# Optimization experiments

Hardware: AMD Instinct MI355X
Metric: run time of the kernel (lower is better)

## Reference

```python
import jax, jax.numpy as jnp
import numpy as np

N = 50000
E = 800000
F_IN = 256
HID = 64
HEADS = 4
CLASSES = 32
NEG_SLOPE = 0.2


def setup_inputs() -> dict:
    key = jax.random.key(0)
    ks = jax.random.split(key, 10)
    x = jax.random.normal(ks[0], (N, F_IN), dtype=jnp.float32)
    edge_index = jax.random.randint(ks[1], (2, E), 0, N, dtype=jnp.int64)
    s1 = 1.0 / np.sqrt(F_IN)
    s2 = 1.0 / np.sqrt(HID * HEADS)
    W1 = jax.random.normal(ks[2], (F_IN, HEADS * HID), dtype=jnp.float32) * s1
    a_src1 = jax.random.normal(ks[3], (HEADS, HID), dtype=jnp.float32) * s1
    a_dst1 = jax.random.normal(ks[4], (HEADS, HID), dtype=jnp.float32) * s1
    b1 = jnp.zeros((HEADS * HID,), dtype=jnp.float32)
    W2 = jax.random.normal(ks[5], (HEADS * HID, CLASSES), dtype=jnp.float32) * s2
    a_src2 = jax.random.normal(ks[6], (1, CLASSES), dtype=jnp.float32) * s2
    a_dst2 = jax.random.normal(ks[7], (1, CLASSES), dtype=jnp.float32) * s2
    b2 = jnp.zeros((CLASSES,), dtype=jnp.float32)
    return {"x": x, "edge_index": edge_index, "W1": W1, "a_src1": a_src1,
            "a_dst1": a_dst1, "b1": b1, "W2": W2, "a_src2": a_src2,
            "a_dst2": a_dst2, "b2": b2}


def gat_conv(x, src, dst, W, a_src, a_dst, bias, num_nodes):
    # PyG GATConv: h = x W, per-head attention logits, segment softmax over dst,
    # scatter-weighted aggregation. src/dst already include self-loops.
    H, C = a_src.shape
    h = (x @ W).reshape(num_nodes, H, C)               # [N, H, C]
    al_s = jnp.sum(h * a_src[None], axis=-1)            # [N, H]
    al_d = jnp.sum(h * a_dst[None], axis=-1)            # [N, H]
    e = jax.nn.leaky_relu(al_s[src] + al_d[dst], NEG_SLOPE)  # [Et, H]
    m = jax.ops.segment_max(e, dst, num_segments=num_nodes)  # [N, H]
    ex = jnp.exp(e - m[dst])
    denom = jax.ops.segment_sum(ex, dst, num_segments=num_nodes)
    alpha = ex / denom[dst]                              # [Et, H]
    out = jax.ops.segment_sum(alpha[:, :, None] * h[src], dst,
                              num_segments=num_nodes)    # [N, H, C]
    return out.reshape(num_nodes, H * C) + bias


def reference(x, edge_index, W1, a_src1, a_dst1, b1, W2, a_src2, a_dst2, b2):
    num_nodes = x.shape[0]
    loop = jnp.arange(num_nodes, dtype=edge_index.dtype)
    src = jnp.concatenate([edge_index[0], loop])  # add_self_loops=True (PyG default)
    dst = jnp.concatenate([edge_index[1], loop])
    # dropout is identity in eval mode
    h = jax.nn.elu(gat_conv(x, src, dst, W1, a_src1, a_dst1, b1, num_nodes))
    out = gat_conv(h, src, dst, W2, a_src2, a_dst2, b2, num_nodes)
    return jax.nn.log_softmax(out, axis=1)
```

## Files before the change

### kernel.cpp

```cpp
#include <hip/hip_runtime.h>
#include <math.h>

#define N_NODES 50000
#define N_EDGES 800000
#define NEG_SLOPE 0.2f
#define PADU N_NODES

#define BSHIFT 8
#define NBUK ((N_NODES + 255) >> BSHIFT)
#define BCAP 4608
#define ACHUNK 4096
#define ET_PAD_ALLOC 1000960

typedef __attribute__((ext_vector_type(8))) short s16x8;
typedef __attribute__((ext_vector_type(4))) float f32x4;
typedef __attribute__((ext_vector_type(2))) float f32x2;

__device__ __forceinline__ unsigned short f2bf(float f) {
    union { float f; unsigned u; } v; v.f = f;
    unsigned r = v.u + 0x7FFF + ((v.u >> 16) & 1);
    return (unsigned short)(r >> 16);
}
__device__ __forceinline__ float bf2f(unsigned short s) {
    union { unsigned u; float f; } v; v.u = ((unsigned)s) << 16;
    return v.f;
}
__device__ __forceinline__ uint4 pack_bf16_trunc(float4 f0, float4 f1) {
    const unsigned* a = (const unsigned*)&f0;
    const unsigned* b = (const unsigned*)&f1;
    uint4 r;
    r.x = (a[0] >> 16) | (a[1] & 0xffff0000u);
    r.y = (a[2] >> 16) | (a[3] & 0xffff0000u);
    r.z = (b[0] >> 16) | (b[1] & 0xffff0000u);
    r.w = (b[2] >> 16) | (b[3] & 0xffff0000u);
    return r;
}
__device__ __forceinline__ unsigned char f2fp8(float f) {
    return (unsigned char)(__builtin_amdgcn_cvt_pk_fp8_f32(f, f, 0, false) & 0xff);
}


__global__ __launch_bounds__(256) void k_cvtw(const float* __restrict__ W1, const float* __restrict__ W2,
                                              unsigned short* __restrict__ WT, unsigned short* __restrict__ W2T,
                                              int* __restrict__ bcur, float* __restrict__ als1) {
    int b = blockIdx.x, k = threadIdx.x;
    if (b < 256) {
        WT[b * 256 + k] = f2bf(W1[k * 256 + b]);
    } else if (b < 288) {
        int c = b - 256;
        W2T[c * 256 + k] = f2bf(W2[k * 32 + c]);
    } else {
        if (k < NBUK) bcur[k] = 0;
        if (k >= 196 && k < 200) als1[N_NODES * 4 + (k - 196)] = -1e30f;
    }
}


__global__ __launch_bounds__(256) void k_bin(const int* __restrict__ ei, int* __restrict__ bcur,
                                             unsigned* __restrict__ stage) {
    __shared__ unsigned sdata[ACHUNK];
    __shared__ unsigned short sv[ACHUNK];
    __shared__ int scnt[NBUK];
    __shared__ int soff[NBUK + 1];
    __shared__ int sgbase[NBUK];
    __shared__ int wssc[4];
    int tid = threadIdx.x;
    int e0 = blockIdx.x * ACHUNK;
    int nE = N_EDGES - e0;
    if (nE > ACHUNK) nE = ACHUNK;
    for (int i = tid; i < NBUK; i += 256) scnt[i] = 0;
    __syncthreads();
    for (int i = tid; i < nE; i += 256) {
        int v = ei[N_EDGES + e0 + i];
        sv[i] = (unsigned short)v;
        atomicAdd(&scnt[v >> BSHIFT], 1);
    }
    __syncthreads();
    {
        int lane = tid & 63, w = tid >> 6;
        int val = (tid < NBUK) ? scnt[tid] : 0;
        int incl = val;
        for (int o = 1; o < 64; o <<= 1) {
            int t = __shfl_up(incl, o);
            if (lane >= o) incl += t;
        }
        if (lane == 63) wssc[w] = incl;
        __syncthreads();
        int wb = 0;
        for (int i = 0; i < w; ++i) wb += wssc[i];
        if (tid < NBUK) soff[tid] = wb + incl - val;
        if (tid == 255) soff[NBUK] = wb + incl;
    }
    __syncthreads();
    if (tid < NBUK) {
        int c = scnt[tid];
        sgbase[tid] = c ? atomicAdd(&bcur[tid], c) : 0;
        scnt[tid] = soff[tid];
    }
    __syncthreads();
    for (int i = tid; i < nE; i += 256) {
        int u = ei[e0 + i];
        unsigned v = sv[i];
        int b = (int)(v >> BSHIFT);
        int pos = atomicAdd(&scnt[b], 1);
        sdata[pos] = (unsigned)u | ((v & 255u) << 16) | ((unsigned)b << 24);
    }
    __syncthreads();
    for (int i = tid; i < nE; i += 256) {
        unsigned pk = sdata[i];
        int buk = (int)(pk >> 24);
        int rel = sgbase[buk] + (i - soff[buk]);
        if (rel < BCAP) stage[(size_t)buk * BCAP + rel] = pk;
    }
}


__global__ __launch_bounds__(256) void k_bukscan(const int* __restrict__ bcur, int* __restrict__ bukbase) {
    __shared__ int ws[4];
    int tid = threadIdx.x, lane = tid & 63, w = tid >> 6;
    int val = 0;
    if (tid < NBUK) {
        int base = tid << BSHIFT;
        int nv = N_NODES - base;
        if (nv > 256) nv = 256;
        val = (bcur[tid] + 4 * nv + 3) & ~3;
    }
    int incl = val;
    for (int o = 1; o < 64; o <<= 1) {
        int t = __shfl_up(incl, o);
        if (lane >= o) incl += t;
    }
    if (lane == 63) ws[w] = incl;
    __syncthreads();
    int wb = 0;
    for (int i = 0; i < w; ++i) wb += ws[i];
    if (tid < NBUK) bukbase[tid] = wb + incl - val;
}


__global__ __launch_bounds__(256) void k_build(const unsigned* __restrict__ stage,
                                               const int* __restrict__ bcur, const int* __restrict__ bukbase,
                                               int* __restrict__ offp, int* __restrict__ ecnt,
                                               unsigned short* __restrict__ esrc) {
    __shared__ int hist[256];
    __shared__ int lexcl[257];
    __shared__ int ws[4];
    __shared__ int outbuf[5632];
    int b = blockIdx.x, tid = threadIdx.x;
    int n = bcur[b];
    if (n > BCAP) n = BCAP;
    int base = b << BSHIFT;
    int nv = N_NODES - base;
    if (nv > 256) nv = 256;
    hist[tid] = 0;
    __syncthreads();
    const unsigned* sg = stage + (size_t)b * BCAP;
    for (int i = tid; i < n; i += 256) atomicAdd(&hist[(sg[i] >> 16) & 0xFF], 1);
    __syncthreads();
    int lane = tid & 63, w = tid >> 6;
    int c = (tid < nv) ? hist[tid] + 1 : 0;
    int r = (tid < nv) ? ((c + 3) & ~3) : 0;
    int incl = r;
    for (int o = 1; o < 64; o <<= 1) {
        int t = __shfl_up(incl, o);
        if (lane >= o) incl += t;
    }
    if (lane == 63) ws[w] = incl;
    __syncthreads();
    int wb = 0;
    for (int i = 0; i < w; ++i) wb += ws[i];
    int excl = wb + incl - r;
    lexcl[tid] = excl;
    if (tid == 255) lexcl[256] = excl + r;
    int gb = bukbase[b];
    if (tid < nv) {
        offp[base + tid] = gb + excl;
        ecnt[base + tid] = c;
    }
    __syncthreads();
    int total = lexcl[256];
    if (tid < nv) {
        outbuf[excl] = base + tid;
        for (int j = excl + c; j < excl + r; ++j) outbuf[j] = PADU;
        hist[tid] = 1;
    }
    __syncthreads();
    for (int i = tid; i < n; i += 256) {
        unsigned pk = sg[i];
        int vloc = (int)((pk >> 16) & 0xFF);
        int pos = lexcl[vloc] + atomicAdd(&hist[vloc], 1);
        outbuf[pos] = (int)(pk & 0xffffu);
    }
    __syncthreads();
    for (int i = tid; i < total; i += 256) esrc[gb + i] = (unsigned short)outbuf[i];
}


__global__ __launch_bounds__(256) void k_gemm1m(const float* __restrict__ X, const unsigned short* __restrict__ WT,
                                                const float* __restrict__ a_src, const float* __restrict__ a_dst,
                                                unsigned char* __restrict__ H8,
                                                float* __restrict__ als, float* __restrict__ ald) {
    __shared__ unsigned short As[64][40];
    __shared__ unsigned short Bs[256][40];
    int tid = threadIdx.x;
    int row0 = blockIdx.x * 64;
    int wv = tid >> 6, lane = tid & 63;
    int wm = wv & 1, wn = wv >> 1;
    int lr = lane & 15, quad = lane >> 4;
    f32x4 acc[2][8];
#pragma unroll
    for (int mt = 0; mt < 2; ++mt)
#pragma unroll
        for (int nt = 0; nt < 8; ++nt) acc[mt][nt] = (f32x4){0.f, 0.f, 0.f, 0.f};

    int ar = tid >> 2, aseg = tid & 3;
    for (int k0 = 0; k0 < 256; k0 += 32) {
        {
            int grow = row0 + ar;
            float4 f0 = make_float4(0.f, 0.f, 0.f, 0.f), f1 = f0;
            if (grow < N_NODES) {
                const float* src = X + (size_t)grow * 256 + k0 + aseg * 8;
                f0 = *(const float4*)src;
                f1 = *(const float4*)(src + 4);
            }
            *(uint4*)&As[ar][aseg * 8] = pack_bf16_trunc(f0, f1);
        }
#pragma unroll
        for (int pass = 0; pass < 4; ++pass) {
            int q = tid + pass * 256;
            int n = q >> 2, seg = q & 3;
            uint4 v = *(const uint4*)(WT + (n << 8) + k0 + seg * 8);
            *(uint4*)&Bs[n][seg * 8] = v;
        }
        __syncthreads();
        s16x8 a[2], b[8];
#pragma unroll
        for (int mt = 0; mt < 2; ++mt) a[mt] = *(const s16x8*)&As[wm * 32 + mt * 16 + lr][quad * 8];
#pragma unroll
        for (int nt = 0; nt < 8; ++nt) b[nt] = *(const s16x8*)&Bs[wn * 128 + nt * 16 + lr][quad * 8];
#pragma unroll
        for (int mt = 0; mt < 2; ++mt)
#pragma unroll
            for (int nt = 0; nt < 8; ++nt)
                acc[mt][nt] = __builtin_amdgcn_mfma_f32_16x16x32_bf16(a[mt], b[nt], acc[mt][nt], 0, 0, 0);
        __syncthreads();
    }
#pragma unroll
    for (int mt = 0; mt < 2; ++mt) {
#pragma unroll
        for (int r = 0; r < 4; ++r) {
            int row = row0 + wm * 32 + mt * 16 + quad * 4 + r;
            if (row < N_NODES) {
#pragma unroll
                for (int nt = 0; nt < 8; ++nt) {
                    int col = wn * 128 + nt * 16 + lr;
                    H8[(size_t)row * 256 + col] = f2fp8(acc[mt][nt][r]);
                }
            }
        }
    }
    float av[8], dv[8];
#pragma unroll
    for (int nt = 0; nt < 8; ++nt) {
        int col = wn * 128 + nt * 16 + lr;
        av[nt] = a_src[col];
        dv[nt] = a_dst[col];
    }
    float ps[2][8], pd[2][8];
#pragma unroll
    for (int hl = 0; hl < 2; ++hl)
#pragma unroll
        for (int i = 0; i < 8; ++i) { ps[hl][i] = 0.f; pd[hl][i] = 0.f; }
#pragma unroll
    for (int mt = 0; mt < 2; ++mt)
#pragma unroll
        for (int nt = 0; nt < 8; ++nt) {
            int hl = nt >> 2;
#pragma unroll
            for (int r = 0; r < 4; ++r) {
                float v = acc[mt][nt][r];
                ps[hl][mt * 4 + r] = fmaf(v, av[nt], ps[hl][mt * 4 + r]);
                pd[hl][mt * 4 + r] = fmaf(v, dv[nt], pd[hl][mt * 4 + r]);
            }
        }
#pragma unroll
    for (int hl = 0; hl < 2; ++hl)
#pragma unroll
        for (int i = 0; i < 8; ++i) {
            float s = ps[hl][i], d = pd[hl][i];
#pragma unroll
            for (int m = 8; m >= 1; m >>= 1) { s += __shfl_xor(s, m); d += __shfl_xor(d, m); }
            if (lr == 0) {
                int row = row0 + wm * 32 + (i >> 2) * 16 + quad * 4 + (i & 3);
                if (row < N_NODES) {
                    als[row * 4 + wn * 2 + hl] = s;
                    ald[row * 4 + wn * 2 + hl] = d;
                }
            }
        }
}


__global__ __launch_bounds__(256) void k_agg1(const unsigned* __restrict__ H8u,
                                              const float* __restrict__ als, const float* __restrict__ ald_,
                                              const int* __restrict__ offp, const int* __restrict__ ecnt,
                                              const unsigned short* __restrict__ esrc,
                                              const float* __restrict__ b1, unsigned* __restrict__ H2p) {
    int wid = (blockIdx.x * 256 + threadIdx.x) >> 6;
    int lane = threadIdx.x & 63;
    int head = lane >> 4;
    float ald = ald_[wid * 4 + head];
    int pstart = offp[wid];
    int rend = pstart + ((ecnt[wid] + 3) & ~3);
    float l = 0.f, ax = 0.f, ay = 0.f, az = 0.f, aw = 0.f;

    auto quad = [&](unsigned ua, unsigned ub) {
        int u0 = (int)(ua & 0xffffu), u1 = (int)(ua >> 16);
        int u2 = (int)(ub & 0xffffu), u3 = (int)(ub >> 16);
        unsigned v0 = H8u[(unsigned)min(u0, N_NODES - 1) * 64 + lane];
        unsigned v1 = H8u[(unsigned)min(u1, N_NODES - 1) * 64 + lane];
        unsigned v2 = H8u[(unsigned)min(u2, N_NODES - 1) * 64 + lane];
        unsigned v3 = H8u[(unsigned)min(u3, N_NODES - 1) * 64 + lane];
        float e0 = als[u0 * 4 + head] + ald;
        float e1 = als[u1 * 4 + head] + ald;
        float e2 = als[u2 * 4 + head] + ald;
        float e3 = als[u3 * 4 + head] + ald;
        e0 = fmaxf(e0, NEG_SLOPE * e0);
        e1 = fmaxf(e1, NEG_SLOPE * e1);
        e2 = fmaxf(e2, NEG_SLOPE * e2);
        e3 = fmaxf(e3, NEG_SLOPE * e3);
        float pw0 = __expf(e0), pw1 = __expf(e1), pw2 = __expf(e2), pw3 = __expf(e3);
        l += (pw0 + pw1) + (pw2 + pw3);
        f32x2 a0 = __builtin_amdgcn_cvt_pk_f32_fp8(v0, false), b0 = __builtin_amdgcn_cvt_pk_f32_fp8(v0, true);
        f32x2 a1 = __builtin_amdgcn_cvt_pk_f32_fp8(v1, false), b1v = __builtin_amdgcn_cvt_pk_f32_fp8(v1, true);
        f32x2 a2 = __builtin_amdgcn_cvt_pk_f32_fp8(v2, false), b2v = __builtin_amdgcn_cvt_pk_f32_fp8(v2, true);
        f32x2 a3 = __builtin_amdgcn_cvt_pk_f32_fp8(v3, false), b3v = __builtin_amdgcn_cvt_pk_f32_fp8(v3, true);
        ax = fmaf(pw3, a3.x, fmaf(pw2, a2.x, fmaf(pw1, a1.x, fmaf(pw0, a0.x, ax))));
        ay = fmaf(pw3, a3.y, fmaf(pw2, a2.y, fmaf(pw1, a1.y, fmaf(pw0, a0.y, ay))));
        az = fmaf(pw3, b3v.x, fmaf(pw2, b2v.x, fmaf(pw1, b1v.x, fmaf(pw0, b0.x, az))));
        aw = fmaf(pw3, b3v.y, fmaf(pw2, b2v.y, fmaf(pw1, b1v.y, fmaf(pw0, b0.y, aw))));
    };

    int p = pstart;
    for (; p + 7 < rend; p += 8) {
        uint2 ua = *(const uint2*)(esrc + p);
        uint2 ub = *(const uint2*)(esrc + p + 4);
        quad(ua.x, ua.y);
        quad(ub.x, ub.y);
    }
    if (p < rend) {
        uint2 ua = *(const uint2*)(esrc + p);
        quad(ua.x, ua.y);
    }

    float inv = 1.f / l;
    int c = lane * 4;
    float4 bb = *(const float4*)(b1 + c);
    float o0 = ax * inv + bb.x, o1 = ay * inv + bb.y, o2 = az * inv + bb.z, o3 = aw * inv + bb.w;
    o0 = o0 > 0.f ? o0 : expm1f(o0);
    o1 = o1 > 0.f ? o1 : expm1f(o1);
    o2 = o2 > 0.f ? o2 : expm1f(o2);
    o3 = o3 > 0.f ? o3 : expm1f(o3);
    unsigned pk = __builtin_amdgcn_cvt_pk_fp8_f32(o0, o1, 0, false);
    pk = __builtin_amdgcn_cvt_pk_fp8_f32(o2, o3, pk, true);
    H2p[(unsigned)wid * 64 + lane] = pk;
}


__global__ __launch_bounds__(256) void k_gemm2m(const unsigned* __restrict__ H2p,
                                                const unsigned short* __restrict__ W2T,
                                                const float* __restrict__ as2, const float* __restrict__ ad2,
                                                unsigned short* __restrict__ Gb, float* __restrict__ als2,
                                                float* __restrict__ ald2) {
    int tid = threadIdx.x;
    int wv = tid >> 6, lane = tid & 63, lr = lane & 15, quad = lane >> 4;
    int row0 = blockIdx.x * 64 + wv * 16;
    int rowA = row0 + lr;
    unsigned rA = (rowA < N_NODES) ? (unsigned)rowA : (unsigned)(N_NODES - 1);
    f32x4 acc[2];
    acc[0] = (f32x4){0.f, 0.f, 0.f, 0.f};
    acc[1] = (f32x4){0.f, 0.f, 0.f, 0.f};
#pragma unroll
    for (int k0 = 0; k0 < 256; k0 += 32) {
        uint2 d = *(const uint2*)(H2p + rA * 64 + (k0 >> 2) + quad * 2);
        f32x2 f0 = __builtin_amdgcn_cvt_pk_f32_fp8(d.x, false);
        f32x2 f1 = __builtin_amdgcn_cvt_pk_f32_fp8(d.x, true);
        f32x2 f2 = __builtin_amdgcn_cvt_pk_f32_fp8(d.y, false);
        f32x2 f3 = __builtin_amdgcn_cvt_pk_f32_fp8(d.y, true);
        union { uint4 u; s16x8 s; } cv;
        cv.u = pack_bf16_trunc(make_float4(f0.x, f0.y, f1.x, f1.y), make_float4(f2.x, f2.y, f3.x, f3.y));
        s16x8 afrag = cv.s;
        s16x8 b0 = *(const s16x8*)(W2T + lr * 256 + k0 + quad * 8);
        s16x8 b1f = *(const s16x8*)(W2T + (16 + lr) * 256 + k0 + quad * 8);
        acc[0] = __builtin_amdgcn_mfma_f32_16x16x32_bf16(afrag, b0, acc[0], 0, 0, 0);
        acc[1] = __builtin_amdgcn_mfma_f32_16x16x32_bf16(afrag, b1f, acc[1], 0, 0, 0);
    }
    float a2s = as2[lr], a2s2 = as2[16 + lr];
    float a2d = ad2[lr], a2d2 = ad2[16 + lr];
#pragma unroll
    for (int r = 0; r < 4; ++r) {
        int row = row0 + quad * 4 + r;
        float g0 = acc[0][r], g1 = acc[1][r];
        float s = g0 * a2s + g1 * a2s2;
        float dd = g0 * a2d + g1 * a2d2;
#pragma unroll
        for (int m = 8; m >= 1; m >>= 1) { s += __shfl_xor(s, m); dd += __shfl_xor(dd, m); }
        if (row < N_NODES) {
            Gb[(size_t)row * 32 + lr] = f2bf(g0);
            Gb[(size_t)row * 32 + 16 + lr] = f2bf(g1);
            if (lr == 0) { als2[row] = s; ald2[row] = dd; }
        }
    }
}


__global__ __launch_bounds__(256) void k_agg2(const unsigned short* __restrict__ Gb,
                                              const float* __restrict__ als2,
                                              const float* __restrict__ ald2_, const int* __restrict__ offp,
                                              const int* __restrict__ ecnt,
                                              const unsigned short* __restrict__ esrc, const float* __restrict__ b2,
                                              float* __restrict__ out) {
    int gid = blockIdx.x * 256 + threadIdx.x;
    int node = gid >> 5;
    int col = gid & 31;
    if (node >= N_NODES) return;
    float ald = ald2_[node];
    int pstart = offp[node];
    int pend = pstart + ecnt[node];
    float l = 0.f, acc = 0.f;

    auto edge1 = [&](int u0) {
        float g0 = bf2f(Gb[(size_t)(unsigned)u0 * 32 + col]);
        float e0 = als2[u0] + ald;
        e0 = fmaxf(e0, NEG_SLOPE * e0);
        float pw0 = __expf(e0);
        l += pw0;
        acc = fmaf(pw0, g0, acc);
    };
    auto quad = [&](unsigned ua, unsigned ub) {
        int u0 = (int)(ua & 0xffffu), u1 = (int)(ua >> 16);
        int u2 = (int)(ub & 0xffffu), u3 = (int)(ub >> 16);
        float g0 = bf2f(Gb[(size_t)(unsigned)u0 * 32 + col]);
        float g1 = bf2f(Gb[(size_t)(unsigned)u1 * 32 + col]);
        float g2 = bf2f(Gb[(size_t)(unsigned)u2 * 32 + col]);
        float g3 = bf2f(Gb[(size_t)(unsigned)u3 * 32 + col]);
        float e0 = als2[u0] + ald, e1 = als2[u1] + ald, e2 = als2[u2] + ald, e3 = als2[u3] + ald;
        e0 = fmaxf(e0, NEG_SLOPE * e0); e1 = fmaxf(e1, NEG_SLOPE * e1);
        e2 = fmaxf(e2, NEG_SLOPE * e2); e3 = fmaxf(e3, NEG_SLOPE * e3);
        float pw0 = __expf(e0), pw1 = __expf(e1), pw2 = __expf(e2), pw3 = __expf(e3);
        l += (pw0 + pw1) + (pw2 + pw3);
        acc = fmaf(pw3, g3, fmaf(pw2, g2, fmaf(pw1, g1, fmaf(pw0, g0, acc))));
    };

    int p = pstart;
    for (; p + 7 < pend; p += 8) {
        uint2 ua = *(const uint2*)(esrc + p);
        uint2 ub = *(const uint2*)(esrc + p + 4);
        quad(ua.x, ua.y);
        quad(ub.x, ub.y);
    }
    for (; p + 3 < pend; p += 4) {
        uint2 ua = *(const uint2*)(esrc + p);
        quad(ua.x, ua.y);
    }
    for (; p < pend; ++p) edge1(esrc[p]);

    float o = acc / l + b2[col];
    float mm = o;
#pragma unroll
    for (int msk = 16; msk >= 1; msk >>= 1) mm = fmaxf(mm, __shfl_xor(mm, msk));
    float ex = __expf(o - mm);
    float s = ex;
#pragma unroll
    for (int msk = 16; msk >= 1; msk >>= 1) s += __shfl_xor(s, msk);
    out[(size_t)node * 32 + col] = o - mm - logf(s);
}


extern "C" void kernel_launch(void* const* d_in, const int* in_sizes, int n_in,
                              void* d_out, int out_size, void* d_ws, size_t ws_size,
                              hipStream_t stream) {
    const float* x   = (const float*)d_in[0];
    const int*   ei  = (const int*)d_in[1];
    const float* W1  = (const float*)d_in[2];
    const float* as1 = (const float*)d_in[3];
    const float* ad1 = (const float*)d_in[4];
    const float* b1  = (const float*)d_in[5];
    const float* W2  = (const float*)d_in[6];
    const float* as2 = (const float*)d_in[7];
    const float* ad2 = (const float*)d_in[8];
    const float* b2  = (const float*)d_in[9];
    float* out = (float*)d_out;

    char* p = (char*)d_ws;
    auto alloc = [&](size_t bytes) {
        char* r = p;
        p += (bytes + 255) & ~(size_t)255;
        return r;
    };
    unsigned char*  h8  = (unsigned char*)alloc((size_t)N_NODES * 256);
    unsigned char*  h2pr= (unsigned char*)alloc((size_t)N_NODES * 64 * 4);
    unsigned short* wt  = (unsigned short*)alloc((size_t)256 * 256 * 2);
    unsigned short* w2t = (unsigned short*)alloc((size_t)32 * 256 * 2);
    float* als1 = (float*)alloc(((size_t)N_NODES * 4 + 4) * 4);
    float* ald1 = (float*)alloc((size_t)N_NODES * 4 * 4);
    float* als2 = (float*)alloc((size_t)N_NODES * 4);
    float* ald2 = (float*)alloc((size_t)N_NODES * 4);
    int* bcur    = (int*)alloc(256 * 4);
    int* bukbase = (int*)alloc(256 * 4);
    int* offp = (int*)alloc((size_t)N_NODES * 4);
    int* ecnt = (int*)alloc((size_t)N_NODES * 4);
    unsigned short* esrc = (unsigned short*)alloc((size_t)ET_PAD_ALLOC * 2);

    unsigned* stage = (unsigned*)h2pr;
    unsigned* h2p = (unsigned*)h2pr;
    unsigned short* g = (unsigned short*)h8;

    k_cvtw<<<289, 256, 0, stream>>>(W1, W2, wt, w2t, bcur, als1);
    k_bin<<<(N_EDGES + ACHUNK - 1) / ACHUNK, 256, 0, stream>>>(ei, bcur, stage);
    k_bukscan<<<1, 256, 0, stream>>>(bcur, bukbase);
    k_build<<<NBUK, 256, 0, stream>>>(stage, bcur, bukbase, offp, ecnt, esrc);

    k_gemm1m<<<(N_NODES + 63) / 64, 256, 0, stream>>>(x, wt, as1, ad1, h8, als1, ald1);
    k_agg1<<<N_NODES / 4, 256, 0, stream>>>((const unsigned*)h8, als1, ald1, offp, ecnt, esrc, b1, h2p);
    k_gemm2m<<<(N_NODES + 63) / 64, 256, 0, stream>>>(h2p, w2t, as2, ad2, g, als2, ald2);
    k_agg2<<<(N_NODES * 32 + 255) / 256, 256, 0, stream>>>(g, als2, ald2, offp, ecnt, esrc, b2, out);
}
```

Before: 227.1 us.

## Fold log2e into attention logits, use exp2, pack aggregation math, halve agg2 threads

Attention coefficient vectors are pre-scaled by log2(e) in both GEMM epilogues, so the aggregation kernels can call the hardware exp2 directly instead of __expf. In agg1 the clamp on padded source indices is replaced by a zeroed padding row appended to H8, and accumulation uses packed f32x2 math. agg2 now gives each thread two output columns through a packed bf16x2 load and float2 store, halving the thread count and the shuffle reductions. These changes cut ALU and instruction count in the gather loops. In exchange each agg2 thread does more serial work and there are fewer waves to hide gather latency.

```diff
diff --git a/kernel.cpp b/kernel.cpp
--- a/kernel.cpp
+++ b/kernel.cpp
@@ -5,6 +5,7 @@
 #define N_EDGES 800000
 #define NEG_SLOPE 0.2f
 #define PADU N_NODES
+#define LOG2E 1.44269504088896f
 
 #define BSHIFT 8
 #define NBUK ((N_NODES + 255) >> BSHIFT)
@@ -21,8 +22,8 @@
     unsigned r = v.u + 0x7FFF + ((v.u >> 16) & 1);
     return (unsigned short)(r >> 16);
 }
-__device__ __forceinline__ float bf2f(unsigned short s) {
-    union { unsigned u; float f; } v; v.u = ((unsigned)s) << 16;
+__device__ __forceinline__ float asf(unsigned u) {
+    union { unsigned u; float f; } v; v.u = u;
     return v.f;
 }
 __device__ __forceinline__ uint4 pack_bf16_trunc(float4 f0, float4 f1) {
@@ -42,7 +43,8 @@
 
 __global__ __launch_bounds__(256) void k_cvtw(const float* __restrict__ W1, const float* __restrict__ W2,
                                               unsigned short* __restrict__ WT, unsigned short* __restrict__ W2T,
-                                              int* __restrict__ bcur, float* __restrict__ als1) {
+                                              int* __restrict__ bcur, float* __restrict__ als1,
+                                              unsigned char* __restrict__ H8) {
     int b = blockIdx.x, k = threadIdx.x;
     if (b < 256) {
         WT[b * 256 + k] = f2bf(W1[k * 256 + b]);
@@ -52,6 +54,7 @@
     } else {
         if (k < NBUK) bcur[k] = 0;
         if (k >= 196 && k < 200) als1[N_NODES * 4 + (k - 196)] = -1e30f;
+        if (k >= 200 && k < 264) ((unsigned*)(H8 + (size_t)N_NODES * 256))[k - 200] = 0;
     }
 }
 
@@ -263,8 +266,8 @@
 #pragma unroll
     for (int nt = 0; nt < 8; ++nt) {
         int col = wn * 128 + nt * 16 + lr;
-        av[nt] = a_src[col];
-        dv[nt] = a_dst[col];
+        av[nt] = a_src[col] * LOG2E;
+        dv[nt] = a_dst[col] * LOG2E;
     }
     float ps[2][8], pd[2][8];
 #pragma unroll
@@ -312,33 +315,38 @@
     float ald = ald_[wid * 4 + head];
     int pstart = offp[wid];
     int rend = pstart + ((ecnt[wid] + 3) & ~3);
-    float l = 0.f, ax = 0.f, ay = 0.f, az = 0.f, aw = 0.f;
+    float l = 0.f;
+    f32x2 axy = (f32x2){0.f, 0.f}, azw = (f32x2){0.f, 0.f};
 
     auto quad = [&](unsigned ua, unsigned ub) {
         int u0 = (int)(ua & 0xffffu), u1 = (int)(ua >> 16);
         int u2 = (int)(ub & 0xffffu), u3 = (int)(ub >> 16);
-        unsigned v0 = H8u[(unsigned)min(u0, N_NODES - 1) * 64 + lane];
-        unsigned v1 = H8u[(unsigned)min(u1, N_NODES - 1) * 64 + lane];
-        unsigned v2 = H8u[(unsigned)min(u2, N_NODES - 1) * 64 + lane];
-        unsigned v3 = H8u[(unsigned)min(u3, N_NODES - 1) * 64 + lane];
-        float e0 = als[u0 * 4 + head] + ald;
-        float e1 = als[u1 * 4 + head] + ald;
-        float e2 = als[u2 * 4 + head] + ald;
-        float e3 = als[u3 * 4 + head] + ald;
-        e0 = fmaxf(e0, NEG_SLOPE * e0);
-        e1 = fmaxf(e1, NEG_SLOPE * e1);
-        e2 = fmaxf(e2, NEG_SLOPE * e2);
-        e3 = fmaxf(e3, NEG_SLOPE * e3);
-        float pw0 = __expf(e0), pw1 = __expf(e1), pw2 = __expf(e2), pw3 = __expf(e3);
+        unsigned v0 = H8u[(unsigned)u0 * 64 + lane];
+        unsigned v1 = H8u[(unsigned)u1 * 64 + lane];
+        unsigned v2 = H8u[(unsigned)u2 * 64 + lane];
+        unsigned v3 = H8u[(unsigned)u3 * 64 + lane];
+        f32x2 e01 = (f32x2){als[u0 * 4 + head], als[u1 * 4 + head]} + (f32x2){ald, ald};
+        f32x2 e23 = (f32x2){als[u2 * 4 + head], als[u3 * 4 + head]} + (f32x2){ald, ald};
+        f32x2 t01 = e01 * NEG_SLOPE, t23 = e23 * NEG_SLOPE;
+        float e0 = fmaxf(e01.x, t01.x), e1 = fmaxf(e01.y, t01.y);
+        float e2 = fmaxf(e23.x, t23.x), e3 = fmaxf(e23.y, t23.y);
+        float pw0 = __builtin_amdgcn_exp2f(e0);
+        float pw1 = __builtin_amdgcn_exp2f(e1);
+        float pw2 = __builtin_amdgcn_exp2f(e2);
+        float pw3 = __builtin_amdgcn_exp2f(e3);
         l += (pw0 + pw1) + (pw2 + pw3);
         f32x2 a0 = __builtin_amdgcn_cvt_pk_f32_fp8(v0, false), b0 = __builtin_amdgcn_cvt_pk_f32_fp8(v0, true);
         f32x2 a1 = __builtin_amdgcn_cvt_pk_f32_fp8(v1, false), b1v = __builtin_amdgcn_cvt_pk_f32_fp8(v1, true);
         f32x2 a2 = __builtin_amdgcn_cvt_pk_f32_fp8(v2, false), b2v = __builtin_amdgcn_cvt_pk_f32_fp8(v2, true);
         f32x2 a3 = __builtin_amdgcn_cvt_pk_f32_fp8(v3, false), b3v = __builtin_amdgcn_cvt_pk_f32_fp8(v3, true);
-        ax = fmaf(pw3, a3.x, fmaf(pw2, a2.x, fmaf(pw1, a1.x, fmaf(pw0, a0.x, ax))));
-        ay = fmaf(pw3, a3.y, fmaf(pw2, a2.y, fmaf(pw1, a1.y, fmaf(pw0, a0.y, ay))));
-        az = fmaf(pw3, b3v.x, fmaf(pw2, b2v.x, fmaf(pw1, b1v.x, fmaf(pw0, b0.x, az))));
-        aw = fmaf(pw3, b3v.y, fmaf(pw2, b2v.y, fmaf(pw1, b1v.y, fmaf(pw0, b0.y, aw))));
+        axy += (f32x2){pw0, pw0} * a0;
+        azw += (f32x2){pw0, pw0} * b0;
+        axy += (f32x2){pw1, pw1} * a1;
+        azw += (f32x2){pw1, pw1} * b1v;
+        axy += (f32x2){pw2, pw2} * a2;
+        azw += (f32x2){pw2, pw2} * b2v;
+        axy += (f32x2){pw3, pw3} * a3;
+        azw += (f32x2){pw3, pw3} * b3v;
     };
 
     int p = pstart;
@@ -356,7 +364,7 @@
     float inv = 1.f / l;
     int c = lane * 4;
     float4 bb = *(const float4*)(b1 + c);
-    float o0 = ax * inv + bb.x, o1 = ay * inv + bb.y, o2 = az * inv + bb.z, o3 = aw * inv + bb.w;
+    float o0 = axy.x * inv + bb.x, o1 = axy.y * inv + bb.y, o2 = azw.x * inv + bb.z, o3 = azw.y * inv + bb.w;
     o0 = o0 > 0.f ? o0 : expm1f(o0);
     o1 = o1 > 0.f ? o1 : expm1f(o1);
     o2 = o2 > 0.f ? o2 : expm1f(o2);
@@ -395,8 +403,8 @@
         acc[0] = __builtin_amdgcn_mfma_f32_16x16x32_bf16(afrag, b0, acc[0], 0, 0, 0);
         acc[1] = __builtin_amdgcn_mfma_f32_16x16x32_bf16(afrag, b1f, acc[1], 0, 0, 0);
     }
-    float a2s = as2[lr], a2s2 = as2[16 + lr];
-    float a2d = ad2[lr], a2d2 = ad2[16 + lr];
+    float a2s = as2[lr] * LOG2E, a2s2 = as2[16 + lr] * LOG2E;
+    float a2d = ad2[lr] * LOG2E, a2d2 = ad2[16 + lr] * LOG2E;
 #pragma unroll
     for (int r = 0; r < 4; ++r) {
         int row = row0 + quad * 4 + r;
@@ -421,35 +429,47 @@
                                               const unsigned short* __restrict__ esrc, const float* __restrict__ b2,
                                               float* __restrict__ out) {
     int gid = blockIdx.x * 256 + threadIdx.x;
-    int node = gid >> 5;
-    int col = gid & 31;
+    int node = gid >> 4;
+    int colp = gid & 15;
     if (node >= N_NODES) return;
     float ald = ald2_[node];
     int pstart = offp[node];
     int pend = pstart + ecnt[node];
-    float l = 0.f, acc = 0.f;
+    float l = 0.f;
+    f32x2 accv = (f32x2){0.f, 0.f};
 
     auto edge1 = [&](int u0) {
-        float g0 = bf2f(Gb[(size_t)(unsigned)u0 * 32 + col]);
+        unsigned gpk = *(const unsigned*)(Gb + (size_t)(unsigned)u0 * 32 + 2 * colp);
+        f32x2 g01 = (f32x2){asf(gpk << 16), asf(gpk & 0xffff0000u)};
         float e0 = als2[u0] + ald;
         e0 = fmaxf(e0, NEG_SLOPE * e0);
-        float pw0 = __expf(e0);
+        float pw0 = __builtin_amdgcn_exp2f(e0);
         l += pw0;
-        acc = fmaf(pw0, g0, acc);
+        accv += (f32x2){pw0, pw0} * g01;
     };
     auto quad = [&](unsigned ua, unsigned ub) {
         int u0 = (int)(ua & 0xffffu), u1 = (int)(ua >> 16);
         int u2 = (int)(ub & 0xffffu), u3 = (int)(ub >> 16);
-        float g0 = bf2f(Gb[(size_t)(unsigned)u0 * 32 + col]);
-        float g1 = bf2f(Gb[(size_t)(unsigned)u1 * 32 + col]);
-        float g2 = bf2f(Gb[(size_t)(unsigned)u2 * 32 + col]);
-        float g3 = bf2f(Gb[(size_t)(unsigned)u3 * 32 + col]);
-        float e0 = als2[u0] + ald, e1 = als2[u1] + ald, e2 = als2[u2] + ald, e3 = als2[u3] + ald;
-        e0 = fmaxf(e0, NEG_SLOPE * e0); e1 = fmaxf(e1, NEG_SLOPE * e1);
-        e2 = fmaxf(e2, NEG_SLOPE * e2); e3 = fmaxf(e3, NEG_SLOPE * e3);
-        float pw0 = __expf(e0), pw1 = __expf(e1), pw2 = __expf(e2), pw3 = __expf(e3);
+        unsigned g0p = *(const unsigned*)(Gb + (size_t)(unsigned)u0 * 32 + 2 * colp);
+        unsigned g1p = *(const unsigned*)(Gb + (size_t)(unsigned)u1 * 32 + 2 * colp);
+        unsigned g2p = *(const unsigned*)(Gb + (size_t)(unsigned)u2 * 32 + 2 * colp);
+        unsigned g3p = *(const unsigned*)(Gb + (size_t)(unsigned)u3 * 32 + 2 * colp);
+        f32x2 e01 = (f32x2){als2[u0], als2[u1]} + (f32x2){ald, ald};
+        f32x2 e23 = (f32x2){als2[u2], als2[u3]} + (f32x2){ald, ald};
+        f32x2 t01 = e01 * NEG_SLOPE, t23 = e23 * NEG_SLOPE;
+        float e0 = fmaxf(e01.x, t01.x), e1 = fmaxf(e01.y, t01.y);
+        float e2 = fmaxf(e23.x, t23.x), e3 = fmaxf(e23.y, t23.y);
+        float pw0 = __builtin_amdgcn_exp2f(e0), pw1 = __builtin_amdgcn_exp2f(e1);
+        float pw2 = __builtin_amdgcn_exp2f(e2), pw3 = __builtin_amdgcn_exp2f(e3);
         l += (pw0 + pw1) + (pw2 + pw3);
-        acc = fmaf(pw3, g3, fmaf(pw2, g2, fmaf(pw1, g1, fmaf(pw0, g0, acc))));
+        f32x2 g0 = (f32x2){asf(g0p << 16), asf(g0p & 0xffff0000u)};
+        f32x2 g1 = (f32x2){asf(g1p << 16), asf(g1p & 0xffff0000u)};
+        f32x2 g2 = (f32x2){asf(g2p << 16), asf(g2p & 0xffff0000u)};
+        f32x2 g3 = (f32x2){asf(g3p << 16), asf(g3p & 0xffff0000u)};
+        accv += (f32x2){pw0, pw0} * g0;
+        accv += (f32x2){pw1, pw1} * g1;
+        accv += (f32x2){pw2, pw2} * g2;
+        accv += (f32x2){pw3, pw3} * g3;
     };
 
     int p = pstart;
@@ -465,15 +485,19 @@
     }
     for (; p < pend; ++p) edge1(esrc[p]);
 
-    float o = acc / l + b2[col];
-    float mm = o;
-#pragma unroll
-    for (int msk = 16; msk >= 1; msk >>= 1) mm = fmaxf(mm, __shfl_xor(mm, msk));
-    float ex = __expf(o - mm);
-    float s = ex;
-#pragma unroll
-    for (int msk = 16; msk >= 1; msk >>= 1) s += __shfl_xor(s, msk);
-    out[(size_t)node * 32 + col] = o - mm - logf(s);
+    float inv = 1.f / l;
+    float2 bb = *(const float2*)(b2 + 2 * colp);
+    float o0 = accv.x * inv + bb.x;
+    float o1 = accv.y * inv + bb.y;
+    float mm = fmaxf(o0, o1);
+#pragma unroll
+    for (int msk = 8; msk >= 1; msk >>= 1) mm = fmaxf(mm, __shfl_xor(mm, msk));
+    float s = __expf(o0 - mm) + __expf(o1 - mm);
+#pragma unroll
+    for (int msk = 8; msk >= 1; msk >>= 1) s += __shfl_xor(s, msk);
+    float ls = logf(s);
+    float2 res = make_float2(o0 - mm - ls, o1 - mm - ls);
+    *(float2*)(out + (size_t)node * 32 + 2 * colp) = res;
 }
 
 
@@ -498,7 +522,7 @@
         p += (bytes + 255) & ~(size_t)255;
         return r;
     };
-    unsigned char*  h8  = (unsigned char*)alloc((size_t)N_NODES * 256);
+    unsigned char*  h8  = (unsigned char*)alloc((size_t)(N_NODES + 1) * 256);
     unsigned char*  h2pr= (unsigned char*)alloc((size_t)N_NODES * 64 * 4);
     unsigned short* wt  = (unsigned short*)alloc((size_t)256 * 256 * 2);
     unsigned short* w2t = (unsigned short*)alloc((size_t)32 * 256 * 2);
@@ -516,7 +540,7 @@
     unsigned* h2p = (unsigned*)h2pr;
     unsigned short* g = (unsigned short*)h8;
 
-    k_cvtw<<<289, 256, 0, stream>>>(W1, W2, wt, w2t, bcur, als1);
+    k_cvtw<<<289, 256, 0, stream>>>(W1, W2, wt, w2t, bcur, als1, h8);
     k_bin<<<(N_EDGES + ACHUNK - 1) / ACHUNK, 256, 0, stream>>>(ei, bcur, stage);
     k_bukscan<<<1, 256, 0, stream>>>(bcur, bukbase);
     k_build<<<NBUK, 256, 0, stream>>>(stage, bcur, bukbase, offp, ecnt, esrc);
@@ -524,5 +548,5 @@
     k_gemm1m<<<(N_NODES + 63) / 64, 256, 0, stream>>>(x, wt, as1, ad1, h8, als1, ald1);
     k_agg1<<<N_NODES / 4, 256, 0, stream>>>((const unsigned*)h8, als1, ald1, offp, ecnt, esrc, b1, h2p);
     k_gemm2m<<<(N_NODES + 63) / 64, 256, 0, stream>>>(h2p, w2t, as2, ad2, g, als2, ald2);
-    k_agg2<<<(N_NODES * 32 + 255) / 256, 256, 0, stream>>>(g, als2, ald2, offp, ecnt, esrc, b2, out);
-}
+    k_agg2<<<(N_NODES * 16 + 255) / 256, 256, 0, stream>>>(g, als2, ald2, offp, ecnt, esrc, b2, out);
+}
```

New measurement: 222.9 us. No clear change (-1.8%).
